# Kernel optimization log

Hardware: AMD Instinct MI355X
Metric: run time of the kernel (lower is better)

The kernel has to match this reference:

```python
import jax, jax.numpy as jnp
import numpy as np

N_REF = 10000
N_QUERY = 10000
N_BATCH = 4
COORD_RANGE = 20.0
INF = jnp.float32(1e30)


def setup_inputs() -> dict:
    key = jax.random.key(0)
    k1, k2, k3, k4 = jax.random.split(key, 4)
    ref_xyz = jax.random.uniform(k1, (N_REF, 3), dtype=jnp.float32) * COORD_RANGE
    ref_b = jax.random.randint(k2, (N_REF, 1), 0, N_BATCH).astype(jnp.float32)
    query_xyz = jax.random.uniform(k3, (N_QUERY, 3), dtype=jnp.float32) * COORD_RANGE
    query_b = jax.random.randint(k4, (N_QUERY, 1), 0, N_BATCH).astype(jnp.float32)
    ref = jnp.concatenate([ref_b, ref_xyz], axis=1)      # [N, 4] (batch, x, y, z)
    query = jnp.concatenate([query_b, query_xyz], axis=1)  # [M, 4]
    return {"ref": ref, "query": query, "radius": 2, "num_neighbors": 32,
            "sort_by_dist": 1}


def _radius_knn(ref, query, radius, num_neighbors, sort_by_dist):
    """Per-query up-to-K neighbors within radius, same batch. Returns [M,K] ref indices (-1 pad)."""
    r2 = jnp.float32(float(radius) ** 2)
    q_xyz, r_xyz = query[:, 1:], ref[:, 1:]
    # squared distances via ||q||^2 + ||r||^2 - 2 q.r  -> avoids [M,N,3] intermediate
    d2 = (jnp.sum(q_xyz * q_xyz, -1)[:, None]
          + jnp.sum(r_xyz * r_xyz, -1)[None, :]
          - 2.0 * q_xyz @ r_xyz.T)                      # [M, N]
    d2 = jnp.maximum(d2, 0.0)
    same_batch = query[:, 0:1] == ref[None, :, 0]       # [M, N]
    valid = same_batch & (d2 <= r2)
    if sort_by_dist:
        sort_key = jnp.where(valid, d2, INF)
    else:  # keep first-encountered refs (deterministic stand-in for hash-bucket order)
        sort_key = jnp.where(valid, jnp.arange(ref.shape[0], dtype=jnp.float32)[None, :], INF)
    neg_key, idx = jax.lax.top_k(-sort_key, num_neighbors)  # smallest keys -> [M, K]
    corres = jnp.where(neg_key > -INF * 0.5, idx, -1)
    return corres


def reference(ref, query, radius, num_neighbors, sort_by_dist):
    corres = _radius_knn(ref, query, radius, num_neighbors, sort_by_dist)  # [M, K]
    M = query.shape[0]
    qidx = jnp.broadcast_to(jnp.arange(M)[:, None], (M, num_neighbors))
    flat = corres.reshape(-1)
    # padded edge list [2, M*K]: row0 = ref idx, row1 = query idx, -1 where no edge
    edges = jnp.stack([flat, jnp.where(flat >= 0, qidx.reshape(-1), -1)], axis=0)
    return edges
```

## Files before the change

kernel.cpp:

```cpp
#include <hip/hip_runtime.h>
#include <cstdint>

typedef unsigned long long u64;

#define KNN_K 32
#define CAP 256
#define WPB 4

#define NB 4
#define GX 10
#define NCELLS (NB*GX*GX*GX)
#define INV_CS 0.5f
#define CELL_CAP 40

#define WS_CNT    0x00000
#define WS_CELLS  0x10000

__device__ __forceinline__ float decode_scalar_f(const int* p) {
    int vi = p[0];
    if (vi >= -1000000 && vi <= 1000000) return (float)vi;
    return __int_as_float(vi);
}

__device__ __forceinline__ int cell_of(float b, float x, float y, float z) {
    int bi = (int)b;
    if (bi < 0 || bi >= NB) return -1;
    int cx = min(GX - 1, max(0, (int)(x * INV_CS)));
    int cy = min(GX - 1, max(0, (int)(y * INV_CS)));
    int cz = min(GX - 1, max(0, (int)(z * INV_CS)));
    return ((bi * GX + cz) * GX + cy) * GX + cx;
}

__global__ void k_build(const float* __restrict__ ref, int* __restrict__ cnt,
                        float4* __restrict__ cells, int N) {
    int i = blockIdx.x * 256 + threadIdx.x;
    if (i < N) {
        float4 rv = *(const float4*)(ref + (size_t)i * 4);
        int c = cell_of(rv.x, rv.y, rv.z, rv.w);
        if (c >= 0) {
            int pos = atomicAdd(cnt + c, 1);
            if (pos < CELL_CAP)
                cells[(size_t)c * CELL_CAP + pos] =
                    make_float4(rv.y, rv.z, rv.w, __int_as_float(i));
        }
    }
}

__global__ __launch_bounds__(256) void k_query2(
    const float* __restrict__ query, const int* __restrict__ cnt,
    const float4* __restrict__ cells, const int* __restrict__ radius_p,
    const int* __restrict__ sbd_p, int* __restrict__ out, int M)
{
#pragma clang fp contract(off)
    __shared__ u64 list[WPB][CAP];
    __shared__ u64 outk[WPB][KNN_K];
    __shared__ int cbase[WPB][64];
    __shared__ int cpre[WPB][64];

    const int w    = threadIdx.x >> 6;
    const int lane = threadIdx.x & 63;
    const int q    = blockIdx.x * WPB + w;
    const u64 SENT = ~0ull;

    const float radf = decode_scalar_f(radius_p);
    const float r2   = radf * radf;
    const bool  sbd  = (sbd_p[0] != 0);
    const int   R    = (int)ceilf(radf * INV_CS);

    unsigned ccount = 0;
    int T = 0;

    float qb = 0.f, q1 = 0.f, q2 = 0.f, q3 = 0.f, qq = 0.f;

    if (q < M) {
        qb = query[q * 4 + 0];
        q1 = query[q * 4 + 1];
        q2 = query[q * 4 + 2];
        q3 = query[q * 4 + 3];
        qq = (q1 * q1 + q2 * q2) + q3 * q3;

        const int bi  = (int)qb;
        const int qcx = min(GX - 1, max(0, (int)(q1 * INV_CS)));
        const int qcy = min(GX - 1, max(0, (int)(q2 * INV_CS)));
        const int qcz = min(GX - 1, max(0, (int)(q3 * INV_CS)));

        const int side = 2 * R + 1;
        int nnb = side * side * side;
        if (nnb > 64) nnb = 64;

        int myCnt = 0, myBase = -1;
        if (lane < nnb && bi >= 0 && bi < NB) {
            const int dz = lane / (side * side) - R;
            const int rm = lane % (side * side);
            const int dy = rm / side - R;
            const int dx = rm % side - R;
            const int cz = qcz + dz, cy = qcy + dy, cx = qcx + dx;
            if ((unsigned)cz < GX && (unsigned)cy < GX && (unsigned)cx < GX) {
                const int cid = ((bi * GX + cz) * GX + cy) * GX + cx;
                myCnt  = min(cnt[cid], CELL_CAP);
                myBase = cid * CELL_CAP;
            }
        }
        int inc = myCnt;
        for (int off = 1; off < 64; off <<= 1) {
            int t = __shfl_up(inc, off);
            if (lane >= off) inc += t;
        }
        T = __shfl(inc, 63);
        cpre[w][lane]  = inc - myCnt;
        cbase[w][lane] = myBase;

        for (int i0 = 0; i0 < T; i0 += 64) {
            const int i = i0 + lane;
            bool valid = false;
            u64 key = 0;
            if (i < T) {
                int lo = 0, hi = nnb - 1;
                while (lo < hi) {
                    const int mid = (lo + hi + 1) >> 1;
                    if (cpre[w][mid] <= i) lo = mid; else hi = mid - 1;
                }
                const int slot = i - cpre[w][lo];
                const float4 p = cells[(size_t)cbase[w][lo] + slot];
                const float rr  = (p.x * p.x + p.y * p.y) + p.z * p.z;
                const float dot = __builtin_fmaf(q3, p.z,
                                   __builtin_fmaf(q2, p.y, q1 * p.x));
                float d2 = (qq + rr) - 2.0f * dot;
                d2 = fmaxf(d2, 0.0f);
                valid = (d2 <= r2);
                const unsigned ridx = (unsigned)__float_as_int(p.w);
                const unsigned hi32 = sbd ? __float_as_uint(d2) : ridx;
                key = ((u64)hi32 << 32) | ridx;
            }
            const u64 mask = __ballot(valid);
            if (valid) {
                const unsigned pos = ccount +
                    (unsigned)__popcll(mask & ((1ull << lane) - 1ull));
                if (pos < CAP) list[w][pos] = key;
            }
            ccount += (unsigned)__popcll(mask);
        }
        if (lane < KNN_K) outk[w][lane] = SENT;
    }
    __syncthreads();

    if (q < M) {
        const int C = (ccount < CAP) ? (int)ccount : CAP;
        for (int i = lane; i < C; i += 64) {
            const u64 ki = list[w][i];
            int rank = 0;
            for (int j = 0; j < C; ++j) rank += (list[w][j] < ki) ? 1 : 0;
            if (rank < KNN_K) outk[w][rank] = ki;
        }
    }
    __syncthreads();

    if (q < M && lane < KNN_K) {
        const u64 key  = outk[w][lane];
        const int ridx = (key == SENT) ? -1 : (int)(unsigned)(key & 0xffffffffull);
        out[(size_t)q * KNN_K + lane] = ridx;
        out[(size_t)M * KNN_K + (size_t)q * KNN_K + lane] = (key == SENT) ? -1 : q;
    }
}

__global__ __launch_bounds__(256) void radius_knn_brute(
    const float* __restrict__ ref, const float* __restrict__ query,
    const int* __restrict__ radius_p, const int* __restrict__ sbd_p,
    int* __restrict__ out, int N, int M)
{
#pragma clang fp contract(off)
    __shared__ u64 list[WPB][CAP];
    __shared__ u64 outk[WPB][KNN_K];

    const int w    = threadIdx.x >> 6;
    const int lane = threadIdx.x & 63;
    const int q    = blockIdx.x * WPB + w;
    const u64 SENT = ~0ull;

    const float radf = decode_scalar_f(radius_p);
    const float r2   = radf * radf;
    const bool  sbd  = (sbd_p[0] != 0);

    unsigned cnt = 0;

    if (q < M) {
        const float qb = query[q * 4 + 0];
        const float q1 = query[q * 4 + 1];
        const float q2 = query[q * 4 + 2];
        const float q3 = query[q * 4 + 3];
        const float qq = (q1 * q1 + q2 * q2) + q3 * q3;

        for (int base = 0; base < N; base += 64) {
            const int r = base + lane;
            bool valid = false;
            u64 key = 0;
            if (r < N) {
                const float4 rv = *(const float4*)(ref + (size_t)r * 4);
                const float rr  = (rv.y * rv.y + rv.z * rv.z) + rv.w * rv.w;
                const float dot = __builtin_fmaf(q3, rv.w,
                                   __builtin_fmaf(q2, rv.z, q1 * rv.y));
                float d2 = (qq + rr) - 2.0f * dot;
                d2 = fmaxf(d2, 0.0f);
                valid = (rv.x == qb) && (d2 <= r2);
                const unsigned hi = sbd ? __float_as_uint(d2) : (unsigned)r;
                key = ((u64)hi << 32) | (unsigned)r;
            }
            const u64 mask = __ballot(valid);
            if (valid) {
                const unsigned pos = cnt + (unsigned)__popcll(mask & ((1ull << lane) - 1ull));
                if (pos < CAP) list[w][pos] = key;
            }
            cnt += (unsigned)__popcll(mask);
        }
        if (lane < KNN_K) outk[w][lane] = SENT;
    }
    __syncthreads();

    if (q < M) {
        const int C = (cnt < CAP) ? (int)cnt : CAP;
        for (int i = lane; i < C; i += 64) {
            const u64 ki = list[w][i];
            int rank = 0;
            for (int j = 0; j < C; ++j) rank += (list[w][j] < ki) ? 1 : 0;
            if (rank < KNN_K) outk[w][rank] = ki;
        }
    }
    __syncthreads();

    if (q < M && lane < KNN_K) {
        const u64 key  = outk[w][lane];
        const int ridx = (key == SENT) ? -1 : (int)(unsigned)(key & 0xffffffffull);
        out[(size_t)q * KNN_K + lane] = ridx;
        out[(size_t)M * KNN_K + (size_t)q * KNN_K + lane] = (key == SENT) ? -1 : q;
    }
}

extern "C" void kernel_launch(void* const* d_in, const int* in_sizes, int n_in,
                              void* d_out, int out_size, void* d_ws, size_t ws_size,
                              hipStream_t stream) {
    const float* ref      = (const float*)d_in[0];
    const float* query    = (const float*)d_in[1];
    const int*   radius_p = (const int*)d_in[2];
    const int*   sbd_p    = (const int*)d_in[4];
    int* out = (int*)d_out;

    const int N = in_sizes[0] / 4;
    const int M = in_sizes[1] / 4;

    const size_t ws_needed = (size_t)WS_CELLS + (size_t)NCELLS * CELL_CAP * 16;
    if (ws_size < ws_needed) {
        radius_knn_brute<<<(M + WPB - 1) / WPB, 256, 0, stream>>>(
            ref, query, radius_p, sbd_p, out, N, M);
        return;
    }

    char* ws = (char*)d_ws;
    int*    cnt   = (int*)   (ws + WS_CNT);
    float4* cells = (float4*)(ws + WS_CELLS);

    hipMemsetAsync(cnt, 0, (size_t)NCELLS * sizeof(int), stream);
    k_build<<<(N + 255) / 256, 256, 0, stream>>>(ref, cnt, cells, N);
    k_query2<<<(M + WPB - 1) / WPB, 256, 0, stream>>>(query, cnt, cells,
                                                      radius_p, sbd_p, out, M);
}
```

Measured before the change: 72.69 us.

## Fuse memset, grid build and query into one cooperative persistent kernel

```diff
diff --git a/kernel.cpp b/kernel.cpp
--- a/kernel.cpp
+++ b/kernel.cpp
@@ -1,10 +1,12 @@
 #include <hip/hip_runtime.h>
+#include <hip/hip_cooperative_groups.h>
 #include <cstdint>
 
+namespace cg = cooperative_groups;
 typedef unsigned long long u64;
 
 #define KNN_K 32
-#define CAP 256
+#define CAP 128
 #define WPB 4
 
 #define NB 4
@@ -12,6 +14,8 @@
 #define NCELLS (NB*GX*GX*GX)
 #define INV_CS 0.5f
 #define CELL_CAP 40
+
+#define GRID_BLOCKS 1024
 
 #define WS_CNT    0x00000
 #define WS_CELLS  0x10000
@@ -31,10 +35,21 @@
     return ((bi * GX + cz) * GX + cy) * GX + cx;
 }
 
-__global__ void k_build(const float* __restrict__ ref, int* __restrict__ cnt,
-                        float4* __restrict__ cells, int N) {
-    int i = blockIdx.x * 256 + threadIdx.x;
-    if (i < N) {
+__global__ __launch_bounds__(256, 4) void k_fused(
+    const float* __restrict__ ref, const float* __restrict__ query,
+    const int* __restrict__ radius_p, const int* __restrict__ sbd_p,
+    int* __restrict__ cnt, float4* __restrict__ cells,
+    int* __restrict__ out, int N, int M)
+{
+#pragma clang fp contract(off)
+    cg::grid_group grid = cg::this_grid();
+    const int tid = blockIdx.x * 256 + threadIdx.x;
+    const int nth = gridDim.x * 256;
+
+    for (int i = tid; i < NCELLS; i += nth) cnt[i] = 0;
+    grid.sync();
+
+    for (int i = tid; i < N; i += nth) {
         float4 rv = *(const float4*)(ref + (size_t)i * 4);
         int c = cell_of(rv.x, rv.y, rv.z, rv.w);
         if (c >= 0) {
@@ -44,14 +59,8 @@
                     make_float4(rv.y, rv.z, rv.w, __int_as_float(i));
         }
     }
-}
-
-__global__ __launch_bounds__(256) void k_query2(
-    const float* __restrict__ query, const int* __restrict__ cnt,
-    const float4* __restrict__ cells, const int* __restrict__ radius_p,
-    const int* __restrict__ sbd_p, int* __restrict__ out, int M)
-{
-#pragma clang fp contract(off)
+    grid.sync();
+
     __shared__ u64 list[WPB][CAP];
     __shared__ u64 outk[WPB][KNN_K];
     __shared__ int cbase[WPB][64];
@@ -59,25 +68,21 @@
 
     const int w    = threadIdx.x >> 6;
     const int lane = threadIdx.x & 63;
-    const int q    = blockIdx.x * WPB + w;
     const u64 SENT = ~0ull;
 
     const float radf = decode_scalar_f(radius_p);
     const float r2   = radf * radf;
     const bool  sbd  = (sbd_p[0] != 0);
     const int   R    = (int)ceilf(radf * INV_CS);
-
-    unsigned ccount = 0;
-    int T = 0;
-
-    float qb = 0.f, q1 = 0.f, q2 = 0.f, q3 = 0.f, qq = 0.f;
-
-    if (q < M) {
-        qb = query[q * 4 + 0];
-        q1 = query[q * 4 + 1];
-        q2 = query[q * 4 + 2];
-        q3 = query[q * 4 + 3];
-        qq = (q1 * q1 + q2 * q2) + q3 * q3;
+    const int   QG   = (M + WPB - 1) / WPB;
+
+    for (int qg = blockIdx.x; qg < QG; qg += gridDim.x) {
+        const int q = qg * WPB + w;
+        if (q >= M) continue;
+
+        const float4 qv = *(const float4*)(query + (size_t)q * 4);
+        const float qb = qv.x, q1 = qv.y, q2 = qv.z, q3 = qv.w;
+        const float qq = (q1 * q1 + q2 * q2) + q3 * q3;
 
         const int bi  = (int)qb;
         const int qcx = min(GX - 1, max(0, (int)(q1 * INV_CS)));
@@ -106,10 +111,11 @@
             int t = __shfl_up(inc, off);
             if (lane >= off) inc += t;
         }
-        T = __shfl(inc, 63);
+        const int T = __shfl(inc, 63);
         cpre[w][lane]  = inc - myCnt;
         cbase[w][lane] = myBase;
 
+        unsigned ccount = 0;
         for (int i0 = 0; i0 < T; i0 += 64) {
             const int i = i0 + lane;
             bool valid = false;
@@ -140,11 +146,8 @@
             }
             ccount += (unsigned)__popcll(mask);
         }
+
         if (lane < KNN_K) outk[w][lane] = SENT;
-    }
-    __syncthreads();
-
-    if (q < M) {
         const int C = (ccount < CAP) ? (int)ccount : CAP;
         for (int i = lane; i < C; i += 64) {
             const u64 ki = list[w][i];
@@ -152,10 +155,130 @@
             for (int j = 0; j < C; ++j) rank += (list[w][j] < ki) ? 1 : 0;
             if (rank < KNN_K) outk[w][rank] = ki;
         }
-    }
-    __syncthreads();
-
-    if (q < M && lane < KNN_K) {
+
+        if (lane < KNN_K) {
+            const u64 key  = outk[w][lane];
+            const int ridx = (key == SENT) ? -1 : (int)(unsigned)(key & 0xffffffffull);
+            out[(size_t)q * KNN_K + lane] = ridx;
+            out[(size_t)M * KNN_K + (size_t)q * KNN_K + lane] = (key == SENT) ? -1 : q;
+        }
+    }
+}
+
+__global__ void k_build(const float* __restrict__ ref, int* __restrict__ cnt,
+                        float4* __restrict__ cells, int N) {
+    int i = blockIdx.x * 256 + threadIdx.x;
+    if (i < N) {
+        float4 rv = *(const float4*)(ref + (size_t)i * 4);
+        int c = cell_of(rv.x, rv.y, rv.z, rv.w);
+        if (c >= 0) {
+            int pos = atomicAdd(cnt + c, 1);
+            if (pos < CELL_CAP)
+                cells[(size_t)c * CELL_CAP + pos] =
+                    make_float4(rv.y, rv.z, rv.w, __int_as_float(i));
+        }
+    }
+}
+
+__global__ __launch_bounds__(256) void k_query2(
+    const float* __restrict__ query, const int* __restrict__ cnt,
+    const float4* __restrict__ cells, const int* __restrict__ radius_p,
+    const int* __restrict__ sbd_p, int* __restrict__ out, int M)
+{
+#pragma clang fp contract(off)
+    __shared__ u64 list[WPB][CAP];
+    __shared__ u64 outk[WPB][KNN_K];
+    __shared__ int cbase[WPB][64];
+    __shared__ int cpre[WPB][64];
+
+    const int w    = threadIdx.x >> 6;
+    const int lane = threadIdx.x & 63;
+    const int q    = blockIdx.x * WPB + w;
+    const u64 SENT = ~0ull;
+    if (q >= M) return;
+
+    const float radf = decode_scalar_f(radius_p);
+    const float r2   = radf * radf;
+    const bool  sbd  = (sbd_p[0] != 0);
+    const int   R    = (int)ceilf(radf * INV_CS);
+
+    const float4 qv = *(const float4*)(query + (size_t)q * 4);
+    const float qb = qv.x, q1 = qv.y, q2 = qv.z, q3 = qv.w;
+    const float qq = (q1 * q1 + q2 * q2) + q3 * q3;
+
+    const int bi  = (int)qb;
+    const int qcx = min(GX - 1, max(0, (int)(q1 * INV_CS)));
+    const int qcy = min(GX - 1, max(0, (int)(q2 * INV_CS)));
+    const int qcz = min(GX - 1, max(0, (int)(q3 * INV_CS)));
+
+    const int side = 2 * R + 1;
+    int nnb = side * side * side;
+    if (nnb > 64) nnb = 64;
+
+    int myCnt = 0, myBase = -1;
+    if (lane < nnb && bi >= 0 && bi < NB) {
+        const int dz = lane / (side * side) - R;
+        const int rm = lane % (side * side);
+        const int dy = rm / side - R;
+        const int dx = rm % side - R;
+        const int cz = qcz + dz, cy = qcy + dy, cx = qcx + dx;
+        if ((unsigned)cz < GX && (unsigned)cy < GX && (unsigned)cx < GX) {
+            const int cid = ((bi * GX + cz) * GX + cy) * GX + cx;
+            myCnt  = min(cnt[cid], CELL_CAP);
+            myBase = cid * CELL_CAP;
+        }
+    }
+    int inc = myCnt;
+    for (int off = 1; off < 64; off <<= 1) {
+        int t = __shfl_up(inc, off);
+        if (lane >= off) inc += t;
+    }
+    const int T = __shfl(inc, 63);
+    cpre[w][lane]  = inc - myCnt;
+    cbase[w][lane] = myBase;
+
+    unsigned ccount = 0;
+    for (int i0 = 0; i0 < T; i0 += 64) {
+        const int i = i0 + lane;
+        bool valid = false;
+        u64 key = 0;
+        if (i < T) {
+            int lo = 0, hi = nnb - 1;
+            while (lo < hi) {
+                const int mid = (lo + hi + 1) >> 1;
+                if (cpre[w][mid] <= i) lo = mid; else hi = mid - 1;
+            }
+            const int slot = i - cpre[w][lo];
+            const float4 p = cells[(size_t)cbase[w][lo] + slot];
+            const float rr  = (p.x * p.x + p.y * p.y) + p.z * p.z;
+            const float dot = __builtin_fmaf(q3, p.z,
+                               __builtin_fmaf(q2, p.y, q1 * p.x));
+            float d2 = (qq + rr) - 2.0f * dot;
+            d2 = fmaxf(d2, 0.0f);
+            valid = (d2 <= r2);
+            const unsigned ridx = (unsigned)__float_as_int(p.w);
+            const unsigned hi32 = sbd ? __float_as_uint(d2) : ridx;
+            key = ((u64)hi32 << 32) | ridx;
+        }
+        const u64 mask = __ballot(valid);
+        if (valid) {
+            const unsigned pos = ccount +
+                (unsigned)__popcll(mask & ((1ull << lane) - 1ull));
+            if (pos < CAP) list[w][pos] = key;
+        }
+        ccount += (unsigned)__popcll(mask);
+    }
+
+    if (lane < KNN_K) outk[w][lane] = SENT;
+    const int C = (ccount < CAP) ? (int)ccount : CAP;
+    for (int i = lane; i < C; i += 64) {
+        const u64 ki = list[w][i];
+        int rank = 0;
+        for (int j = 0; j < C; ++j) rank += (list[w][j] < ki) ? 1 : 0;
+        if (rank < KNN_K) outk[w][rank] = ki;
+    }
+
+    if (lane < KNN_K) {
         const u64 key  = outk[w][lane];
         const int ridx = (key == SENT) ? -1 : (int)(unsigned)(key & 0xffffffffull);
         out[(size_t)q * KNN_K + lane] = ridx;
@@ -176,58 +299,52 @@
     const int lane = threadIdx.x & 63;
     const int q    = blockIdx.x * WPB + w;
     const u64 SENT = ~0ull;
+    if (q >= M) return;
 
     const float radf = decode_scalar_f(radius_p);
     const float r2   = radf * radf;
     const bool  sbd  = (sbd_p[0] != 0);
 
     unsigned cnt = 0;
-
-    if (q < M) {
-        const float qb = query[q * 4 + 0];
-        const float q1 = query[q * 4 + 1];
-        const float q2 = query[q * 4 + 2];
-        const float q3 = query[q * 4 + 3];
-        const float qq = (q1 * q1 + q2 * q2) + q3 * q3;
-
-        for (int base = 0; base < N; base += 64) {
-            const int r = base + lane;
-            bool valid = false;
-            u64 key = 0;
-            if (r < N) {
-                const float4 rv = *(const float4*)(ref + (size_t)r * 4);
-                const float rr  = (rv.y * rv.y + rv.z * rv.z) + rv.w * rv.w;
-                const float dot = __builtin_fmaf(q3, rv.w,
-                                   __builtin_fmaf(q2, rv.z, q1 * rv.y));
-                float d2 = (qq + rr) - 2.0f * dot;
-                d2 = fmaxf(d2, 0.0f);
-                valid = (rv.x == qb) && (d2 <= r2);
-                const unsigned hi = sbd ? __float_as_uint(d2) : (unsigned)r;
-                key = ((u64)hi << 32) | (unsigned)r;
-            }
-            const u64 mask = __ballot(valid);
-            if (valid) {
-                const unsigned pos = cnt + (unsigned)__popcll(mask & ((1ull << lane) - 1ull));
-                if (pos < CAP) list[w][pos] = key;
-            }
-            cnt += (unsigned)__popcll(mask);
-        }
-        if (lane < KNN_K) outk[w][lane] = SENT;
-    }
-    __syncthreads();
-
-    if (q < M) {
-        const int C = (cnt < CAP) ? (int)cnt : CAP;
-        for (int i = lane; i < C; i += 64) {
-            const u64 ki = list[w][i];
-            int rank = 0;
-            for (int j = 0; j < C; ++j) rank += (list[w][j] < ki) ? 1 : 0;
-            if (rank < KNN_K) outk[w][rank] = ki;
-        }
-    }
-    __syncthreads();
-
-    if (q < M && lane < KNN_K) {
+    const float qb = query[q * 4 + 0];
+    const float q1 = query[q * 4 + 1];
+    const float q2 = query[q * 4 + 2];
+    const float q3 = query[q * 4 + 3];
+    const float qq = (q1 * q1 + q2 * q2) + q3 * q3;
+
+    for (int base = 0; base < N; base += 64) {
+        const int r = base + lane;
+        bool valid = false;
+        u64 key = 0;
+        if (r < N) {
+            const float4 rv = *(const float4*)(ref + (size_t)r * 4);
+            const float rr  = (rv.y * rv.y + rv.z * rv.z) + rv.w * rv.w;
+            const float dot = __builtin_fmaf(q3, rv.w,
+                               __builtin_fmaf(q2, rv.z, q1 * rv.y));
+            float d2 = (qq + rr) - 2.0f * dot;
+            d2 = fmaxf(d2, 0.0f);
+            valid = (rv.x == qb) && (d2 <= r2);
+            const unsigned hi = sbd ? __float_as_uint(d2) : (unsigned)r;
+            key = ((u64)hi << 32) | (unsigned)r;
+        }
+        const u64 mask = __ballot(valid);
+        if (valid) {
+            const unsigned pos = cnt + (unsigned)__popcll(mask & ((1ull << lane) - 1ull));
+            if (pos < CAP) list[w][pos] = key;
+        }
+        cnt += (unsigned)__popcll(mask);
+    }
+
+    if (lane < KNN_K) outk[w][lane] = SENT;
+    const int C = (cnt < CAP) ? (int)cnt : CAP;
+    for (int i = lane; i < C; i += 64) {
+        const u64 ki = list[w][i];
+        int rank = 0;
+        for (int j = 0; j < C; ++j) rank += (list[w][j] < ki) ? 1 : 0;
+        if (rank < KNN_K) outk[w][rank] = ki;
+    }
+
+    if (lane < KNN_K) {
         const u64 key  = outk[w][lane];
         const int ridx = (key == SENT) ? -1 : (int)(unsigned)(key & 0xffffffffull);
         out[(size_t)q * KNN_K + lane] = ridx;
@@ -244,8 +361,8 @@
     const int*   sbd_p    = (const int*)d_in[4];
     int* out = (int*)d_out;
 
-    const int N = in_sizes[0] / 4;
-    const int M = in_sizes[1] / 4;
+    int N = in_sizes[0] / 4;
+    int M = in_sizes[1] / 4;
 
     const size_t ws_needed = (size_t)WS_CELLS + (size_t)NCELLS * CELL_CAP * 16;
     if (ws_size < ws_needed) {
@@ -258,8 +375,15 @@
     int*    cnt   = (int*)   (ws + WS_CNT);
     float4* cells = (float4*)(ws + WS_CELLS);
 
-    hipMemsetAsync(cnt, 0, (size_t)NCELLS * sizeof(int), stream);
-    k_build<<<(N + 255) / 256, 256, 0, stream>>>(ref, cnt, cells, N);
-    k_query2<<<(M + WPB - 1) / WPB, 256, 0, stream>>>(query, cnt, cells,
-                                                      radius_p, sbd_p, out, M);
-}
+    void* kargs[] = { (void*)&ref, (void*)&query, (void*)&radius_p, (void*)&sbd_p,
+                      (void*)&cnt, (void*)&cells, (void*)&out, (void*)&N, (void*)&M };
+    hipError_t e = hipLaunchCooperativeKernel((const void*)k_fused,
+                                              dim3(GRID_BLOCKS), dim3(256),
+                                              kargs, 0, stream);
+    if (e != hipSuccess) {
+        hipMemsetAsync(cnt, 0, (size_t)NCELLS * sizeof(int), stream);
+        k_build<<<(N + 255) / 256, 256, 0, stream>>>(ref, cnt, cells, N);
+        k_query2<<<(M + WPB - 1) / WPB, 256, 0, stream>>>(query, cnt, cells,
+                                                          radius_p, sbd_p, out, M);
+    }
+}
```

After: 230.7 us. 217% more time.
